# Kernel tuning notes

Hardware: AMD Instinct MI355X
Metric: run time of the kernel (lower is better)

The kernel has to match this reference:

```python
import jax, jax.numpy as jnp
import numpy as np

B, T = 16, 512
LAT, ACT, TSK = 512, 64, 96
E, NH, HD = 1024, 16, 64
L, HID, MAXS = 4, 4096, 512


def setup_inputs() -> dict:
    key = jax.random.key(0)
    ks = jax.random.split(key, 16)
    def rn(k, shape, std=0.02):
        return jax.random.normal(k, shape, jnp.float32) * std
    return {
        "z": jax.random.normal(ks[0], (B, T, LAT), jnp.float32),
        "a": jax.random.normal(ks[1], (B, T, ACT), jnp.float32),
        "task_emb": jax.random.normal(ks[2], (B, T, TSK), jnp.float32),
        "input_proj_w": rn(ks[3], (LAT + ACT + TSK, E)),
        "input_proj_b": jnp.zeros((E,), jnp.float32),
        "pos_emb": rn(ks[4], (1, MAXS, E)),
        "ln1_w": jnp.ones((L, E), jnp.float32),
        "ln1_b": jnp.zeros((L, E), jnp.float32),
        "qkv_w": rn(ks[5], (L, E, 3 * E)),
        "proj_w": rn(ks[6], (L, E, E)),
        "proj_b": jnp.zeros((L, E), jnp.float32),
        "ln2_w": jnp.ones((L, E), jnp.float32),
        "ln2_b": jnp.zeros((L, E), jnp.float32),
        "mlp_w1": rn(ks[7], (L, E, HID)),
        "mlp_b1": jnp.zeros((L, HID), jnp.float32),
        "mlp_w2": rn(ks[8], (L, HID, E)),
        "mlp_b2": jnp.zeros((L, E), jnp.float32),
        "out_norm_w": jnp.ones((E,), jnp.float32),
        "out_norm_b": jnp.zeros((E,), jnp.float32),
        "delta_w": rn(ks[9], (E, LAT)),
        "delta_b": jnp.zeros((LAT,), jnp.float32),
    }


def _ln(x, w, b, eps=1e-5):
    mu = jnp.mean(x, -1, keepdims=True)
    var = jnp.mean((x - mu) ** 2, -1, keepdims=True)
    return (x - mu) * jax.lax.rsqrt(var + eps) * w + b


def reference(z, a, task_emb, input_proj_w, input_proj_b, pos_emb,
              ln1_w, ln1_b, qkv_w, proj_w, proj_b, ln2_w, ln2_b,
              mlp_w1, mlp_b1, mlp_w2, mlp_b2,
              out_norm_w, out_norm_b, delta_w, delta_b):
    Bv, Tv, _ = z.shape
    x = jnp.concatenate([z, a, task_emb], axis=-1) @ input_proj_w + input_proj_b
    x = x + pos_emb[:, :Tv]
    scale = HD ** -0.5
    causal = jnp.tril(jnp.ones((Tv, Tv), bool))  # seq_start=0, no cache
    for l in range(L):
        h = _ln(x, ln1_w[l], ln1_b[l])
        qkv = (h @ qkv_w[l]).reshape(Bv, Tv, 3, NH, HD)
        q = jnp.swapaxes(qkv[:, :, 0], 1, 2) * scale  # (B,H,T,D)
        k = jnp.swapaxes(qkv[:, :, 1], 1, 2)
        v = jnp.swapaxes(qkv[:, :, 2], 1, 2)
        attn = jnp.einsum('bhqd,bhkd->bhqk', q, k)
        attn = jnp.where(causal, attn, -jnp.inf)
        attn = jax.nn.softmax(attn, axis=-1)
        o = jnp.einsum('bhqk,bhkd->bhqd', attn, v)
        o = jnp.swapaxes(o, 1, 2).reshape(Bv, Tv, E)
        x = x + (o @ proj_w[l] + proj_b[l])
        h2 = _ln(x, ln2_w[l], ln2_b[l])
        mid = jax.nn.gelu(h2 @ mlp_w1[l] + mlp_b1[l], approximate=False)
        x = x + (mid @ mlp_w2[l] + mlp_b2[l])
    x = _ln(x, out_norm_w, out_norm_b)
    return z + (x @ delta_w + delta_b)
```

## Files before the change

kernel.cpp:

```cpp
#include <hip/hip_runtime.h>
#include <hip/hip_bf16.h>
#include <math.h>

typedef unsigned short u16;
typedef unsigned int u32;
typedef __attribute__((ext_vector_type(4))) float f32x4;
typedef __attribute__((ext_vector_type(8))) short bf16x8;

#define DEV static __device__ __forceinline__

DEV u16 f2bf(float f) {
  __hip_bfloat16 h = __float2bfloat16(f);
  union { __hip_bfloat16 h; u16 u; } c; c.h = h; return c.u;
}

DEV float fast_gelu(float v) {
  float u = v * (1.5957691216f + 0.0713548162f * v * v);
  return v * __builtin_amdgcn_rcpf(1.f + __expf(-u));
}

DEV void gload16(const void* g, void* l) {
  __builtin_amdgcn_global_load_lds((const __attribute__((address_space(1))) u32*)g,
                                   (__attribute__((address_space(3))) u32*)l, 16, 0, 0);
}

__global__ void transpose_w(const float* __restrict__ src, u16* __restrict__ dst,
                            int R, int C, int Rp) {
  __shared__ float tile[32][33];
  int tx = threadIdx.x, ty = threadIdx.y;
  int c0 = blockIdx.x * 32, r0 = blockIdx.y * 32;
  #pragma unroll
  for (int j = 0; j < 4; j++) {
    int r = r0 + ty + j * 8, c = c0 + tx;
    tile[ty + j * 8][tx] = (r < R && c < C) ? src[(size_t)r * C + c] : 0.f;
  }
  __syncthreads();
  #pragma unroll
  for (int j = 0; j < 4; j++) {
    int cc = c0 + ty + j * 8;
    int rr = r0 + tx;
    if (cc < C && rr < Rp) dst[(size_t)cc * Rp + rr] = f2bf(tile[tx][ty + j * 8]);
  }
}

__global__ void concat_k(const float* __restrict__ z, const float* __restrict__ a,
                         const float* __restrict__ te, u16* __restrict__ A) {
  const int total = 8192 * 704;
  for (int idx = blockIdx.x * 256 + threadIdx.x; idx < total; idx += gridDim.x * 256) {
    int m = idx / 704;
    int j = idx - m * 704;
    float v = 0.f;
    if (j < 512) v = z[(size_t)m * 512 + j];
    else if (j < 576) v = a[(size_t)m * 64 + (j - 512)];
    else if (j < 672) v = te[(size_t)m * 96 + (j - 576)];
    A[idx] = f2bf(v);
  }
}

__global__ __launch_bounds__(256) void ln_k(const float* __restrict__ x,
                                            const float* __restrict__ w,
                                            const float* __restrict__ b,
                                            u16* __restrict__ h) {
  int row = blockIdx.x * 4 + (threadIdx.x >> 6);
  int lane = threadIdx.x & 63;
  const float4* xr = (const float4*)(x + (size_t)row * 1024);
  float4 v[4]; float s = 0.f, sq = 0.f;
  #pragma unroll
  for (int i = 0; i < 4; i++) {
    v[i] = xr[lane + i * 64];
    s += v[i].x + v[i].y + v[i].z + v[i].w;
    sq += v[i].x * v[i].x + v[i].y * v[i].y + v[i].z * v[i].z + v[i].w * v[i].w;
  }
  #pragma unroll
  for (int off = 32; off >= 1; off >>= 1) { s += __shfl_xor(s, off); sq += __shfl_xor(sq, off); }
  float mean = s * (1.f / 1024.f);
  float var = sq * (1.f / 1024.f) - mean * mean;
  float rstd = rsqrtf(var + 1e-5f);
  const float4* wv = (const float4*)w;
  const float4* bv = (const float4*)b;
  u32* hr = (u32*)(h + (size_t)row * 1024);
  #pragma unroll
  for (int i = 0; i < 4; i++) {
    int idx = lane + i * 64;
    float4 wi = wv[idx], bi = bv[idx];
    float o0 = (v[i].x - mean) * rstd * wi.x + bi.x;
    float o1 = (v[i].y - mean) * rstd * wi.y + bi.y;
    float o2 = (v[i].z - mean) * rstd * wi.z + bi.z;
    float o3 = (v[i].w - mean) * rstd * wi.w + bi.w;
    hr[idx * 2]     = (u32)f2bf(o0) | ((u32)f2bf(o1) << 16);
    hr[idx * 2 + 1] = (u32)f2bf(o2) | ((u32)f2bf(o3) << 16);
  }
}

template <int FM, int EPI>
__global__ __launch_bounds__(512, 2) void gemm8(
    const u16* __restrict__ A, const u16* __restrict__ BT,
    float* __restrict__ outF, u16* __restrict__ outH,
    const float* __restrict__ bias, const float* __restrict__ res,
    const float* __restrict__ pos, int M, int N, int K, int gx) {
  constexpr int BM = FM * 32;
  constexpr int ABYTES = BM * 64;
  constexpr int BBYTES = 256 * 64;
  constexpr int SLICE = ABYTES + BBYTES;
  constexpr int LA = ABYTES / 8192;
  constexpr int LB = 2;
  __shared__ char lds[4 * SLICE];

  const int tid = threadIdx.x, lane = tid & 63, w = tid >> 6;
  const int wr = w >> 2, wc = w & 3;

  const int nwg = gridDim.x, orig = blockIdx.x;
  const int q = nwg >> 3, r = nwg & 7;
  const int xcd = orig & 7, loc = orig >> 3;
  const int sid = (xcd < r ? xcd * (q + 1) : r * (q + 1) + (xcd - r) * q) + loc;
  const int m0 = (sid / gx) * BM, n0 = (sid % gx) * 256;

  const char* Ag = (const char*)(A + (size_t)m0 * K);
  const char* Bg = (const char*)(BT + (size_t)n0 * K);
  const int Krow = K * 2;

  int aoff[LA], boff[LB];
  #pragma unroll
  for (int l = 0; l < LA; l++) {
    int c = l * 512 + tid, rw = c >> 2, g = (c & 3) ^ ((rw >> 1) & 3);
    aoff[l] = rw * Krow + g * 16;
  }
  #pragma unroll
  for (int l = 0; l < LB; l++) {
    int c = l * 512 + tid, rw = c >> 2, g = (c & 3) ^ ((rw >> 1) & 3);
    boff[l] = rw * Krow + g * 16;
  }
  const int ra = wr * (FM * 16) + (lane & 15);
  const int aRd = ra * 64 + (((lane >> 4) ^ ((ra >> 1) & 3)) << 4);
  const int rb = wc * 64 + (lane & 15);
  const int bRd = rb * 64 + (((lane >> 4) ^ ((rb >> 1) & 3)) << 4);

  f32x4 zero4 = {0.f, 0.f, 0.f, 0.f};
  f32x4 acc[FM][4];
  #pragma unroll
  for (int m = 0; m < FM; m++)
    #pragma unroll
    for (int n = 0; n < 4; n++) acc[m][n] = zero4;

  auto stageA = [&](int s) {
    char* Ad = lds + (s & 3) * SLICE;
    const char* src = Ag + (size_t)s * 64;
    #pragma unroll
    for (int l = 0; l < LA; l++)
      gload16(src + aoff[l], Ad + (l * 512 + w * 64) * 16);
  };
  auto stageB = [&](int s) {
    char* Bd = lds + (s & 3) * SLICE + ABYTES;
    const char* src = Bg + (size_t)s * 64;
    #pragma unroll
    for (int l = 0; l < LB; l++)
      gload16(src + boff[l], Bd + (l * 512 + w * 64) * 16);
  };

  const int NS = K >> 5;
  stageA(0); stageB(0); stageA(1); stageB(1);
  asm volatile("s_waitcnt vmcnt(3)" ::: "memory");
  __builtin_amdgcn_s_barrier();

  #pragma unroll 1
  for (int s = 0; s < NS; s++) {
    char* Ar = lds + (s & 3) * SLICE;
    char* Br = Ar + ABYTES;
    const bool pre = (s + 2 < NS);
    bf16x8 bfr[4], af[4];
    #pragma unroll
    for (int n = 0; n < 4; n++) bfr[n] = *(const bf16x8*)(Br + bRd + n * 1024);
    #pragma unroll
    for (int m = 0; m < 4; m++) af[m] = *(const bf16x8*)(Ar + aRd + m * 1024);
    if (pre) { stageA(s + 2); stageB(s + 2); }
    __builtin_amdgcn_sched_barrier(0);
    __builtin_amdgcn_s_barrier();
    asm volatile("s_waitcnt lgkmcnt(0)" ::: "memory");
    __builtin_amdgcn_sched_barrier(0);
    __builtin_amdgcn_s_setprio(1);
    #pragma unroll
    for (int m = 0; m < 4; m++)
      #pragma unroll
      for (int n = 0; n < 4; n++)
        acc[m][n] = __builtin_amdgcn_mfma_f32_16x16x32_bf16(af[m], bfr[n], acc[m][n], 0, 0, 0);
    __builtin_amdgcn_s_setprio(0);
    __builtin_amdgcn_sched_barrier(0);
    if (pre) asm volatile("s_waitcnt vmcnt(3)" ::: "memory");
    else     asm volatile("s_waitcnt vmcnt(0)" ::: "memory");
    __builtin_amdgcn_s_barrier();
  }

  #pragma unroll
  for (int m = 0; m < FM; m++) {
    #pragma unroll
    for (int i = 0; i < 4; i++) {
      int gm = m0 + wr * (FM * 16) + m * 16 + ((lane >> 4) << 2) + i;
      #pragma unroll
      for (int n = 0; n < 4; n++) {
        int gn = n0 + wc * 64 + n * 16 + (lane & 15);
        float v = acc[m][n][i];
        if (EPI & 1) v += bias[gn];
        if (EPI & 2) v += pos[(size_t)(gm & 511) * N + gn];
        if (EPI & 4) v += res[(size_t)gm * N + gn];
        if (EPI & 8) v = fast_gelu(v);
        if (EPI & 16) outH[(size_t)gm * N + gn] = f2bf(v);
        else outF[(size_t)gm * N + gn] = v;
      }
    }
  }
}

#define SB0 __builtin_amdgcn_sched_barrier(0)
#define VMW(N) asm volatile("s_waitcnt vmcnt(" #N ")" ::: "memory")
#define PH_TAIL(MFMAS) \
  SB0; __builtin_amdgcn_s_barrier(); \
  asm volatile("s_waitcnt lgkmcnt(0)" ::: "memory"); SB0; \
  __builtin_amdgcn_s_setprio(1); MFMAS; __builtin_amdgcn_s_setprio(0); \
  SB0; __builtin_amdgcn_s_barrier();
#define PH_TAILV(MFMAS, NN) \
  SB0; __builtin_amdgcn_s_barrier(); \
  asm volatile("s_waitcnt lgkmcnt(0)" ::: "memory"); SB0; \
  __builtin_amdgcn_s_setprio(1); MFMAS; __builtin_amdgcn_s_setprio(0); \
  SB0; VMW(NN); __builtin_amdgcn_s_barrier();
#define MM16(MB, BF) \
  _Pragma("unroll") \
  for (int mm = 0; mm < 4; mm++) \
    _Pragma("unroll") \
    for (int nn = 0; nn < 4; nn++) \
      acc[(MB) + mm][nn] = __builtin_amdgcn_mfma_f32_16x16x32_bf16(afr[mm][0], BF[nn], acc[(MB) + mm][nn], 0, 0, 0);
#define MM32(MB) \
  _Pragma("unroll") \
  for (int kk2 = 0; kk2 < 2; kk2++) \
    _Pragma("unroll") \
    for (int mm = 0; mm < 4; mm++) \
      _Pragma("unroll") \
      for (int nn = 0; nn < 4; nn++) \
        acc[(MB) + mm][nn] = __builtin_amdgcn_mfma_f32_16x16x32_bf16( \
            afr[mm][kk2], kk2 ? bfr1[nn] : bfr0[nn], acc[(MB) + mm][nn], 0, 0, 0);
#define RD_A1(BUF, K2L, MB) { \
  const char* _b = aRdB[BUF]; \
  afr[0][0] = *(const bf16x8*)(_b + aby[(MB) + 0][K2L]); \
  afr[1][0] = *(const bf16x8*)(_b + aby[(MB) + 1][K2L]); \
  afr[2][0] = *(const bf16x8*)(_b + aby[(MB) + 2][K2L]); \
  afr[3][0] = *(const bf16x8*)(_b + aby[(MB) + 3][K2L]); }
#define RD_A8(BUF, MB) { \
  const char* _b = aRdB[BUF]; \
  afr[0][0] = *(const bf16x8*)(_b + aby[(MB) + 0][0]); \
  afr[0][1] = *(const bf16x8*)(_b + aby[(MB) + 0][1]); \
  afr[1][0] = *(const bf16x8*)(_b + aby[(MB) + 1][0]); \
  afr[1][1] = *(const bf16x8*)(_b + aby[(MB) + 1][1]); \
  afr[2][0] = *(const bf16x8*)(_b + aby[(MB) + 2][0]); \
  afr[2][1] = *(const bf16x8*)(_b + aby[(MB) + 2][1]); \
  afr[3][0] = *(const bf16x8*)(_b + aby[(MB) + 3][0]); \
  afr[3][1] = *(const bf16x8*)(_b + aby[(MB) + 3][1]); }
#define RD_BALL(BUF) { \
  const char* _b = bRdB[BUF]; \
  bfr0[0] = *(const bf16x8*)(_b + bby[0][0]); bfr1[0] = *(const bf16x8*)(_b + bby[0][1]); \
  bfr0[1] = *(const bf16x8*)(_b + bby[1][0]); bfr1[1] = *(const bf16x8*)(_b + bby[1][1]); \
  bfr0[2] = *(const bf16x8*)(_b + bby[2][0]); bfr1[2] = *(const bf16x8*)(_b + bby[2][1]); \
  bfr0[3] = *(const bf16x8*)(_b + bby[3][0]); bfr1[3] = *(const bf16x8*)(_b + bby[3][1]); }

template <int FM, int EPI>
__global__ __launch_bounds__(512, 2) void gemmP(
    const u16* __restrict__ A, const u16* __restrict__ BT,
    float* __restrict__ outF, u16* __restrict__ outH,
    const float* __restrict__ bias, const float* __restrict__ res,
    const float* __restrict__ pos, int M, int N, int K, int gx) {
  constexpr int RB = 16384;
  constexpr int NAREG = (FM == 8 ? 4 : 2);
  constexpr int BOFF = NAREG * RB;
  __shared__ char lds[BOFF + 4 * RB];

  const int tid = threadIdx.x, lane = tid & 63, w = tid >> 6;
  const int wr = w >> 2, wc = w & 3;
  const int ln = lane & 15, g = lane >> 4;

  const int nwg = gridDim.x, orig = blockIdx.x;
  const int q = nwg >> 3, r = nwg & 7;
  const int xcd = orig & 7, loc = orig >> 3;
  const int sid = (xcd < r ? xcd * (q + 1) : r * (q + 1) + (xcd - r) * q) + loc;
  const int m0 = (sid / gx) * (FM * 32), n0 = (sid % gx) * 256;

  const char* Ag = (const char*)(A + (size_t)m0 * K);
  const char* Bg = (const char*)(BT + (size_t)n0 * K);
  const size_t K2 = (size_t)K * 2;
  const int NT = K >> 6, NTm1 = NT - 1, NI = NT >> 1;

  int aby[FM][2], bby[4][2];
  #pragma unroll
  for (int m = 0; m < FM; m++) {
    int rr = (FM == 8 ? 0 : wr * 64) + m * 16 + ln;
    #pragma unroll
    for (int k2 = 0; k2 < 2; k2++)
      aby[m][k2] = rr * 128 + (((k2 * 4 + g) ^ (rr & 7)) << 4);
  }
  #pragma unroll
  for (int n = 0; n < 4; n++) {
    int rr = (wc & 1) * 64 + n * 16 + ln;
    #pragma unroll
    for (int k2 = 0; k2 < 2; k2++)
      bby[n][k2] = rr * 128 + (((k2 * 4 + g) ^ (rr & 7)) << 4);
  }
  const char* aRdB[2];
  const char* bRdB[2];
  if constexpr (FM == 8) {
    aRdB[0] = lds + (0 * 2 + wr) * RB;
    aRdB[1] = lds + (1 * 2 + wr) * RB;
  } else {
    aRdB[0] = lds;
    aRdB[1] = lds + RB;
  }
  bRdB[0] = lds + BOFF + (0 * 2 + (wc >> 1)) * RB;
  bRdB[1] = lds + BOFF + (1 * 2 + (wc >> 1)) * RB;

  int soff[2], sdst[2];
  #pragma unroll
  for (int l = 0; l < 2; l++) {
    int c = l * 512 + tid, rw = c >> 3, sl = c & 7;
    soff[l] = rw * (int)K2 + ((sl ^ (rw & 7)) << 4);
    sdst[l] = (l * 512 + w * 64) * 16;
  }

  auto stA = [&](int buf, int tau, int h) {
    char* d = lds + (FM == 8 ? (buf * 2 + h) : buf) * RB;
    const char* s = Ag + (size_t)(tau < NT ? tau : NTm1) * 128 + (FM == 8 ? (size_t)h * 128 * K2 : 0);
    #pragma unroll
    for (int l = 0; l < 2; l++) gload16(s + soff[l], d + sdst[l]);
  };
  auto stB = [&](int buf, int tau, int gg) {
    char* d = lds + BOFF + (buf * 2 + gg) * RB;
    const char* s = Bg + (size_t)(tau < NT ? tau : NTm1) * 128 + (size_t)gg * 128 * K2;
    #pragma unroll
    for (int l = 0; l < 2; l++) gload16(s + soff[l], d + sdst[l]);
  };

  f32x4 zero4 = {0.f, 0.f, 0.f, 0.f};
  f32x4 acc[FM][4];
  #pragma unroll
  for (int m = 0; m < FM; m++)
    #pragma unroll
    for (int n = 0; n < 4; n++) acc[m][n] = zero4;

  bf16x8 afr[4][2], bfr0[4], bfr1[4];

  if constexpr (FM == 8) {
    stA(0, 0, 0); stA(0, 0, 1); stB(0, 0, 0); stB(0, 0, 1); stB(1, 1, 0); stB(1, 1, 1);
    VMW(4);
    __builtin_amdgcn_s_barrier();
    #pragma unroll 1
    for (int J = 0; J < NI; J++) {
      const int t = 2 * J;
      RD_BALL(0); RD_A8(0, 0); stA(1, t + 1, 0); stA(1, t + 1, 1);
      PH_TAIL(MM32(0));
      RD_A8(0, 4); stB(0, t + 2, 0); stB(0, t + 2, 1);
      PH_TAILV(MM32(4), 4);
      RD_BALL(1); RD_A8(1, 0); stA(0, t + 2, 0); stA(0, t + 2, 1);
      PH_TAIL(MM32(0));
      RD_A8(1, 4); stB(1, t + 3, 0); stB(1, t + 3, 1);
      PH_TAILV(MM32(4), 4);
    }
  } else {
    stA(0, 0, 0); stB(0, 0, 0); stB(0, 0, 1); stB(1, 1, 0); stB(1, 1, 1);
    VMW(4);
    __builtin_amdgcn_s_barrier();
    #pragma unroll 1
    for (int J = 0; J < NI; J++) {
      const int t = 2 * J;
      RD_BALL(0); RD_A1(0, 0, 0); stA(1, t + 1, 0);
      PH_TAIL(MM16(0, bfr0));
      RD_A1(0, 1, 0); stB(0, t + 2, 0);
      PH_TAILV(MM16(0, bfr1), 2);
      RD_BALL(1); RD_A1(1, 0, 0); stB(0, t + 2, 1); stA(0, t + 2, 0);
      PH_TAIL(MM16(0, bfr0));
      RD_A1(1, 1, 0); stB(1, t + 3, 0); stB(1, t + 3, 1);
      PH_TAILV(MM16(0, bfr1), 4);
    }
  }
  VMW(0);

  #pragma unroll
  for (int m = 0; m < FM; m++) {
    #pragma unroll
    for (int i = 0; i < 4; i++) {
      int gm = m0 + wr * (FM * 16) + m * 16 + (g << 2) + i;
      #pragma unroll
      for (int n = 0; n < 4; n++) {
        int gn = n0 + wc * 64 + n * 16 + ln;
        float v = acc[m][n][i];
        if (EPI & 1) v += bias[gn];
        if (EPI & 2) v += pos[(size_t)(gm & 511) * N + gn];
        if (EPI & 4) v += res[(size_t)gm * N + gn];
        if (EPI & 8) v = fast_gelu(v);
        if (EPI & 16) outH[(size_t)gm * N + gn] = f2bf(v);
        else outF[(size_t)gm * N + gn] = v;
      }
    }
  }
}
#undef RD_BALL
#undef RD_A8
#undef RD_A1
#undef MM32
#undef MM16
#undef PH_TAILV
#undef PH_TAIL
#undef VMW
#undef SB0

__global__ __launch_bounds__(512) void attn_k(const u16* __restrict__ qkv,
                                              u16* __restrict__ o) {
  __shared__ u16 Ks[512 * 64];
  __shared__ u16 Vt[64 * 512];
  __shared__ u16 Ps[8 * 512];
  const int tid = threadIdx.x, lane = tid & 63, w = tid >> 6;
  const int b = blockIdx.x >> 4, h = blockIdx.x & 15;
  const u16* base = qkv + (size_t)b * 512 * 3072 + h * 64;

  #pragma unroll
  for (int it = 0; it < 8; it++) {
    int chunk = it * 512 + tid;
    int row = chunk >> 3;
    int ib = (chunk & 7) * 16;
    int lb = ib ^ ((row & 7) << 4);
    gload16((const char*)(base + 1024 + (size_t)row * 3072) + lb,
            (char*)Ks + (it * 512 + w * 64) * 16);
  }
  {
    const u16* vrow = base + 2048 + (size_t)tid * 3072;
    #pragma unroll
    for (int c = 0; c < 8; c++) {
      uint4 u = *(const uint4*)(vrow + c * 8);
      u32 vals[4] = {u.x, u.y, u.z, u.w};
      #pragma unroll
      for (int pcompo = 0; pcompo < 4; pcompo++) {
        int d0 = c * 8 + pcompo * 2;
        size_t by0 = ((size_t)d0 * 1024 + tid * 2) ^ (size_t)((d0 & 7) << 4);
        size_t by1 = ((size_t)(d0 + 1) * 1024 + tid * 2) ^ (size_t)(((d0 + 1) & 7) << 4);
        *(u16*)((char*)Vt + by0) = (u16)(vals[pcompo] & 0xffff);
        *(u16*)((char*)Vt + by1) = (u16)(vals[pcompo] >> 16);
      }
    }
  }
  __syncthreads();

  const int qts[4] = {w, 15 - w, 16 + w, 31 - w};
  #pragma unroll
  for (int qi = 0; qi < 4; qi++) {
    const int qt = qts[qi];
    const int q0 = qt * 16;
    const int qcol = q0 + (lane & 15);
    const u16* qrow = base + (size_t)(q0 + (lane & 15)) * 3072 + ((lane >> 4) << 3);
    bf16x8 qf0 = *(const bf16x8*)qrow;
    bf16x8 qf1 = *(const bf16x8*)(qrow + 32);
    f32x4 zero4 = {0.f, 0.f, 0.f, 0.f};
    f32x4 oA[4] = {zero4, zero4, zero4, zero4};
    float mrun = -INFINITY, lrun = 0.f;
    const int nch = (qt >> 1) + 1;
    for (int ch = 0; ch < nch; ch++) {
      const int kb = ch * 32;
      f32x4 st0 = zero4, st1 = zero4;
      {
        int krow = kb + (lane & 15);
        int byc = krow * 128 + ((lane >> 4) << 4);
        int sw = (krow & 7) << 4;
        bf16x8 ka = *(const bf16x8*)((const char*)Ks + (byc ^ sw));
        bf16x8 kb2 = *(const bf16x8*)((const char*)Ks + ((byc + 64) ^ sw));
        st0 = __builtin_amdgcn_mfma_f32_16x16x32_bf16(ka, qf0, st0, 0, 0, 0);
        st0 = __builtin_amdgcn_mfma_f32_16x16x32_bf16(kb2, qf1, st0, 0, 0, 0);
      }
      {
        int krow = kb + 16 + (lane & 15);
        int byc = krow * 128 + ((lane >> 4) << 4);
        int sw = (krow & 7) << 4;
        bf16x8 ka = *(const bf16x8*)((const char*)Ks + (byc ^ sw));
        bf16x8 kb2 = *(const bf16x8*)((const char*)Ks + ((byc + 64) ^ sw));
        st1 = __builtin_amdgcn_mfma_f32_16x16x32_bf16(ka, qf0, st1, 0, 0, 0);
        st1 = __builtin_amdgcn_mfma_f32_16x16x32_bf16(kb2, qf1, st1, 0, 0, 0);
      }
      float sv[8]; float cmax = -INFINITY;
      #pragma unroll
      for (int i = 0; i < 4; i++) {
        int key0 = kb + ((lane >> 4) << 2) + i;
        float s0 = st0[i] * 0.125f; if (key0 > qcol) s0 = -INFINITY;
        float s1 = st1[i] * 0.125f; if (key0 + 16 > qcol) s1 = -INFINITY;
        sv[i] = s0; sv[4 + i] = s1;
        cmax = fmaxf(cmax, fmaxf(s0, s1));
      }
      cmax = fmaxf(cmax, __shfl_xor(cmax, 16));
      cmax = fmaxf(cmax, __shfl_xor(cmax, 32));
      float mnew = fmaxf(mrun, cmax);
      float corr = __expf(mrun - mnew);
      float pp[8]; float psum = 0.f;
      #pragma unroll
      for (int i = 0; i < 8; i++) { pp[i] = __expf(sv[i] - mnew); psum += pp[i]; }
      psum += __shfl_xor(psum, 16);
      psum += __shfl_xor(psum, 32);
      lrun = lrun * corr + psum;
      mrun = mnew;
      {
        int rowq = lane & 15;
        int pbase = w * 1024 + rowq * 64;
        int sw = (rowq & 3) << 4;
        uint2 t0, t1;
        t0.x = (u32)f2bf(pp[0]) | ((u32)f2bf(pp[1]) << 16);
        t0.y = (u32)f2bf(pp[2]) | ((u32)f2bf(pp[3]) << 16);
        t1.x = (u32)f2bf(pp[4]) | ((u32)f2bf(pp[5]) << 16);
        t1.y = (u32)f2bf(pp[6]) | ((u32)f2bf(pp[7]) << 16);
        int off0 = (((lane >> 4) << 3)) ^ sw;
        int off1 = (32 + ((lane >> 4) << 3)) ^ sw;
        *(uint2*)((char*)Ps + pbase + off0) = t0;
        *(uint2*)((char*)Ps + pbase + off1) = t1;
      }
      #pragma unroll
      for (int i = 0; i < 4; i++) {
        float fi = __shfl(corr, ((lane >> 4) << 2) + i);
        oA[0][i] *= fi; oA[1][i] *= fi; oA[2][i] *= fi; oA[3][i] *= fi;
      }
      {
        int rowq = lane & 15;
        int pby = w * 1024 + rowq * 64 + ((((lane >> 4) << 4)) ^ ((rowq & 3) << 4));
        bf16x8 pf = *(const bf16x8*)((const char*)Ps + pby);
        #pragma unroll
        for (int n = 0; n < 4; n++) {
          int d = n * 16 + (lane & 15);
          int vby = (d * 1024 + (kb + ((lane >> 4) << 3)) * 2) ^ ((d & 7) << 4);
          bf16x8 vf = *(const bf16x8*)((const char*)Vt + vby);
          oA[n] = __builtin_amdgcn_mfma_f32_16x16x32_bf16(pf, vf, oA[n], 0, 0, 0);
        }
      }
    }
    float inv = 1.f / lrun;
    #pragma unroll
    for (int i = 0; i < 4; i++) {
      float fi = __shfl(inv, ((lane >> 4) << 2) + i);
      int qr = q0 + ((lane >> 4) << 2) + i;
      size_t orow = ((size_t)b * 512 + qr) * 1024 + h * 64;
      #pragma unroll
      for (int n = 0; n < 4; n++)
        o[orow + n * 16 + (lane & 15)] = f2bf(oA[n][i] * fi);
    }
  }
}

extern "C" void kernel_launch(void* const* d_in, const int* in_sizes, int n_in,
                              void* d_out, int out_size, void* d_ws, size_t ws_size,
                              hipStream_t stream) {
  const float* z    = (const float*)d_in[0];
  const float* a    = (const float*)d_in[1];
  const float* te   = (const float*)d_in[2];
  const float* ipw  = (const float*)d_in[3];
  const float* ipb  = (const float*)d_in[4];
  const float* pos  = (const float*)d_in[5];
  const float* ln1w = (const float*)d_in[6];
  const float* ln1b = (const float*)d_in[7];
  const float* qkvw = (const float*)d_in[8];
  const float* projw= (const float*)d_in[9];
  const float* projb= (const float*)d_in[10];
  const float* ln2w = (const float*)d_in[11];
  const float* ln2b = (const float*)d_in[12];
  const float* w1   = (const float*)d_in[13];
  const float* b1   = (const float*)d_in[14];
  const float* w2   = (const float*)d_in[15];
  const float* b2   = (const float*)d_in[16];
  const float* onw  = (const float*)d_in[17];
  const float* onb  = (const float*)d_in[18];
  const float* dw   = (const float*)d_in[19];
  const float* db   = (const float*)d_in[20];
  float* out = (float*)d_out;

  char* p = (char*)d_ws;
  auto alloc = [&](size_t bytes) -> char* {
    char* r = p; p += (bytes + 255) & ~(size_t)255; return r;
  };
  u16* wt_in   = (u16*)alloc((size_t)1024 * 704 * 2);
  u16* wt_qkv  = (u16*)alloc((size_t)4 * 3072 * 1024 * 2);
  u16* wt_proj = (u16*)alloc((size_t)4 * 1024 * 1024 * 2);
  u16* wt_m1   = (u16*)alloc((size_t)4 * 4096 * 1024 * 2);
  u16* wt_m2   = (u16*)alloc((size_t)4 * 1024 * 4096 * 2);
  u16* wt_d    = (u16*)alloc((size_t)512 * 1024 * 2);
  u16* abuf    = (u16*)alloc((size_t)8192 * 704 * 2);
  float* xbuf  = (float*)alloc((size_t)8192 * 1024 * 4);
  u16* hbuf    = (u16*)alloc((size_t)8192 * 1024 * 2);
  u16* big     = (u16*)alloc((size_t)8192 * 4096 * 2);
  u16* obuf    = (u16*)alloc((size_t)8192 * 1024 * 2);
  u16* qkvb = big;
  u16* mid  = big;

  dim3 tb(32, 8);
  auto TR = [&](const float* s, u16* d, int R, int C, int Rp) {
    dim3 g((C + 31) / 32, (Rp + 31) / 32);
    transpose_w<<<g, tb, 0, stream>>>(s, d, R, C, Rp);
  };
  TR(ipw, wt_in, 672, 1024, 704);
  for (int l = 0; l < 4; l++) TR(qkvw + (size_t)l * 1024 * 3072, wt_qkv + (size_t)l * 3072 * 1024, 1024, 3072, 1024);
  for (int l = 0; l < 4; l++) TR(projw + (size_t)l * 1024 * 1024, wt_proj + (size_t)l * 1024 * 1024, 1024, 1024, 1024);
  for (int l = 0; l < 4; l++) TR(w1 + (size_t)l * 1024 * 4096, wt_m1 + (size_t)l * 4096 * 1024, 1024, 4096, 1024);
  for (int l = 0; l < 4; l++) TR(w2 + (size_t)l * 4096 * 1024, wt_m2 + (size_t)l * 1024 * 4096, 4096, 1024, 4096);
  TR(dw, wt_d, 1024, 512, 1024);

  concat_k<<<4096, 256, 0, stream>>>(z, a, te, abuf);

  gemm8<4, 3><<<4 * 64, 512, 0, stream>>>(abuf, wt_in, xbuf, nullptr, ipb, nullptr, pos, 8192, 1024, 704, 4);

  for (int l = 0; l < 4; l++) {
    ln_k<<<2048, 256, 0, stream>>>(xbuf, ln1w + l * 1024, ln1b + l * 1024, hbuf);
    gemmP<8, 16><<<384, 512, 0, stream>>>(hbuf, wt_qkv + (size_t)l * 3072 * 1024, nullptr, qkvb, nullptr, nullptr, nullptr, 8192, 3072, 1024, 12);
    attn_k<<<256, 512, 0, stream>>>(qkvb, obuf);
    gemmP<4, 5><<<256, 512, 0, stream>>>(obuf, wt_proj + (size_t)l * 1024 * 1024, xbuf, nullptr, projb + l * 1024, xbuf, nullptr, 8192, 1024, 1024, 4);
    ln_k<<<2048, 256, 0, stream>>>(xbuf, ln2w + l * 1024, ln2b + l * 1024, hbuf);
    gemmP<8, 25><<<512, 512, 0, stream>>>(hbuf, wt_m1 + (size_t)l * 4096 * 1024, nullptr, mid, b1 + l * 4096, nullptr, nullptr, 8192, 4096, 1024, 16);
    gemmP<4, 5><<<256, 512, 0, stream>>>(mid, wt_m2 + (size_t)l * 1024 * 4096, xbuf, nullptr, b2 + l * 1024, xbuf, nullptr, 8192, 1024, 4096, 4);
  }
  ln_k<<<2048, 256, 0, stream>>>(xbuf, onw, onb, hbuf);
  gemmP<4, 5><<<128, 512, 0, stream>>>(hbuf, wt_d, out, nullptr, db, z, nullptr, 8192, 512, 1024, 2);
}
```

Measured before the change: 1.372 ms.

## Restructure GEMM main loop into two-phase double-buffered pipeline with split LDS waits

Replaces the four-phase-per-iteration GEMM schedule, which had two barriers per phase and B tiles prefetched two steps ahead, with a simpler double-buffered scheme. Each half-iteration now waits on all outstanding global loads, takes a single barrier, issues the next tile's global-to-LDS loads, and reads all A/B fragments for the current tile. A partial lgkmcnt wait lets the first MFMA group start before the second group's fragments arrive. This cuts barrier count and serialisation between phases, but shortens the prefetch distance and adds extra fragment registers (afr1), which risks exposed memory latency or register pressure.

New measurement: 1.375 ms. About the same (+0.2%).

```diff
diff --git a/kernel.cpp b/kernel.cpp
--- a/kernel.cpp
+++ b/kernel.cpp
@@ -211,24 +211,10 @@
 }
 
 #define SB0 __builtin_amdgcn_sched_barrier(0)
-#define VMW(N) asm volatile("s_waitcnt vmcnt(" #N ")" ::: "memory")
-#define PH_TAIL(MFMAS) \
-  SB0; __builtin_amdgcn_s_barrier(); \
-  asm volatile("s_waitcnt lgkmcnt(0)" ::: "memory"); SB0; \
-  __builtin_amdgcn_s_setprio(1); MFMAS; __builtin_amdgcn_s_setprio(0); \
-  SB0; __builtin_amdgcn_s_barrier();
-#define PH_TAILV(MFMAS, NN) \
-  SB0; __builtin_amdgcn_s_barrier(); \
-  asm volatile("s_waitcnt lgkmcnt(0)" ::: "memory"); SB0; \
-  __builtin_amdgcn_s_setprio(1); MFMAS; __builtin_amdgcn_s_setprio(0); \
-  SB0; VMW(NN); __builtin_amdgcn_s_barrier();
-#define MM16(MB, BF) \
-  _Pragma("unroll") \
-  for (int mm = 0; mm < 4; mm++) \
-    _Pragma("unroll") \
-    for (int nn = 0; nn < 4; nn++) \
-      acc[(MB) + mm][nn] = __builtin_amdgcn_mfma_f32_16x16x32_bf16(afr[mm][0], BF[nn], acc[(MB) + mm][nn], 0, 0, 0);
-#define MM32(MB) \
+#define VMW0 asm volatile("s_waitcnt vmcnt(0)" ::: "memory")
+#define LGKM8 asm volatile("s_waitcnt lgkmcnt(8)" ::: "memory")
+#define LGKM0 asm volatile("s_waitcnt lgkmcnt(0)" ::: "memory")
+#define MM32A(AF, MB) \
   _Pragma("unroll") \
   for (int kk2 = 0; kk2 < 2; kk2++) \
     _Pragma("unroll") \
@@ -236,29 +222,38 @@
       _Pragma("unroll") \
       for (int nn = 0; nn < 4; nn++) \
         acc[(MB) + mm][nn] = __builtin_amdgcn_mfma_f32_16x16x32_bf16( \
-            afr[mm][kk2], kk2 ? bfr1[nn] : bfr0[nn], acc[(MB) + mm][nn], 0, 0, 0);
-#define RD_A1(BUF, K2L, MB) { \
-  const char* _b = aRdB[BUF]; \
-  afr[0][0] = *(const bf16x8*)(_b + aby[(MB) + 0][K2L]); \
-  afr[1][0] = *(const bf16x8*)(_b + aby[(MB) + 1][K2L]); \
-  afr[2][0] = *(const bf16x8*)(_b + aby[(MB) + 2][K2L]); \
-  afr[3][0] = *(const bf16x8*)(_b + aby[(MB) + 3][K2L]); }
-#define RD_A8(BUF, MB) { \
-  const char* _b = aRdB[BUF]; \
-  afr[0][0] = *(const bf16x8*)(_b + aby[(MB) + 0][0]); \
-  afr[0][1] = *(const bf16x8*)(_b + aby[(MB) + 0][1]); \
-  afr[1][0] = *(const bf16x8*)(_b + aby[(MB) + 1][0]); \
-  afr[1][1] = *(const bf16x8*)(_b + aby[(MB) + 1][1]); \
-  afr[2][0] = *(const bf16x8*)(_b + aby[(MB) + 2][0]); \
-  afr[2][1] = *(const bf16x8*)(_b + aby[(MB) + 2][1]); \
-  afr[3][0] = *(const bf16x8*)(_b + aby[(MB) + 3][0]); \
-  afr[3][1] = *(const bf16x8*)(_b + aby[(MB) + 3][1]); }
-#define RD_BALL(BUF) { \
+            AF[mm][kk2], kk2 ? bfr1[nn] : bfr0[nn], acc[(MB) + mm][nn], 0, 0, 0);
+#define MM16K(KL) \
+  _Pragma("unroll") \
+  for (int mm = 0; mm < 4; mm++) \
+    _Pragma("unroll") \
+    for (int nn = 0; nn < 4; nn++) \
+      acc[mm][nn] = __builtin_amdgcn_mfma_f32_16x16x32_bf16( \
+          afr0[mm][KL], KL ? bfr1[nn] : bfr0[nn], acc[mm][nn], 0, 0, 0);
+#define RD_B2(BUF) { \
   const char* _b = bRdB[BUF]; \
   bfr0[0] = *(const bf16x8*)(_b + bby[0][0]); bfr1[0] = *(const bf16x8*)(_b + bby[0][1]); \
   bfr0[1] = *(const bf16x8*)(_b + bby[1][0]); bfr1[1] = *(const bf16x8*)(_b + bby[1][1]); \
   bfr0[2] = *(const bf16x8*)(_b + bby[2][0]); bfr1[2] = *(const bf16x8*)(_b + bby[2][1]); \
   bfr0[3] = *(const bf16x8*)(_b + bby[3][0]); bfr1[3] = *(const bf16x8*)(_b + bby[3][1]); }
+#define RD_A4(BUF, MB, DST) { \
+  const char* _b = aRdB[BUF]; \
+  DST[0][0] = *(const bf16x8*)(_b + aby[(MB) + 0][0]); DST[0][1] = *(const bf16x8*)(_b + aby[(MB) + 0][1]); \
+  DST[1][0] = *(const bf16x8*)(_b + aby[(MB) + 1][0]); DST[1][1] = *(const bf16x8*)(_b + aby[(MB) + 1][1]); \
+  DST[2][0] = *(const bf16x8*)(_b + aby[(MB) + 2][0]); DST[2][1] = *(const bf16x8*)(_b + aby[(MB) + 2][1]); \
+  DST[3][0] = *(const bf16x8*)(_b + aby[(MB) + 3][0]); DST[3][1] = *(const bf16x8*)(_b + aby[(MB) + 3][1]); }
+#define RD_BK(BUF, KL, DST4) { \
+  const char* _b = bRdB[BUF]; \
+  DST4[0] = *(const bf16x8*)(_b + bby[0][KL]); \
+  DST4[1] = *(const bf16x8*)(_b + bby[1][KL]); \
+  DST4[2] = *(const bf16x8*)(_b + bby[2][KL]); \
+  DST4[3] = *(const bf16x8*)(_b + bby[3][KL]); }
+#define RD_AK(BUF, KL) { \
+  const char* _b = aRdB[BUF]; \
+  afr0[0][KL] = *(const bf16x8*)(_b + aby[0][KL]); \
+  afr0[1][KL] = *(const bf16x8*)(_b + aby[1][KL]); \
+  afr0[2][KL] = *(const bf16x8*)(_b + aby[2][KL]); \
+  afr0[3][KL] = *(const bf16x8*)(_b + aby[3][KL]); }
 
 template <int FM, int EPI>
 __global__ __launch_bounds__(512, 2) void gemmP(
@@ -341,42 +336,58 @@
     #pragma unroll
     for (int n = 0; n < 4; n++) acc[m][n] = zero4;
 
-  bf16x8 afr[4][2], bfr0[4], bfr1[4];
+  bf16x8 afr0[4][2], afr1[4][2], bfr0[4], bfr1[4];
 
   if constexpr (FM == 8) {
-    stA(0, 0, 0); stA(0, 0, 1); stB(0, 0, 0); stB(0, 0, 1); stB(1, 1, 0); stB(1, 1, 1);
-    VMW(4);
-    __builtin_amdgcn_s_barrier();
+    stA(0, 0, 0); stA(0, 0, 1); stB(0, 0, 0); stB(0, 0, 1);
     #pragma unroll 1
     for (int J = 0; J < NI; J++) {
       const int t = 2 * J;
-      RD_BALL(0); RD_A8(0, 0); stA(1, t + 1, 0); stA(1, t + 1, 1);
-      PH_TAIL(MM32(0));
-      RD_A8(0, 4); stB(0, t + 2, 0); stB(0, t + 2, 1);
-      PH_TAILV(MM32(4), 4);
-      RD_BALL(1); RD_A8(1, 0); stA(0, t + 2, 0); stA(0, t + 2, 1);
-      PH_TAIL(MM32(0));
-      RD_A8(1, 4); stB(1, t + 3, 0); stB(1, t + 3, 1);
-      PH_TAILV(MM32(4), 4);
+      VMW0; SB0;
+      __builtin_amdgcn_s_barrier();
+      stA(1, t + 1, 0); stA(1, t + 1, 1); stB(1, t + 1, 0); stB(1, t + 1, 1);
+      RD_B2(0); RD_A4(0, 0, afr0); SB0;
+      RD_A4(0, 4, afr1); SB0;
+      LGKM8; SB0;
+      __builtin_amdgcn_s_setprio(1); MM32A(afr0, 0); __builtin_amdgcn_s_setprio(0); SB0;
+      LGKM0; SB0;
+      __builtin_amdgcn_s_setprio(1); MM32A(afr1, 4); __builtin_amdgcn_s_setprio(0); SB0;
+      VMW0; SB0;
+      __builtin_amdgcn_s_barrier();
+      stA(0, t + 2, 0); stA(0, t + 2, 1); stB(0, t + 2, 0); stB(0, t + 2, 1);
+      RD_B2(1); RD_A4(1, 0, afr0); SB0;
+      RD_A4(1, 4, afr1); SB0;
+      LGKM8; SB0;
+      __builtin_amdgcn_s_setprio(1); MM32A(afr0, 0); __builtin_amdgcn_s_setprio(0); SB0;
+      LGKM0; SB0;
+      __builtin_amdgcn_s_setprio(1); MM32A(afr1, 4); __builtin_amdgcn_s_setprio(0); SB0;
     }
   } else {
-    stA(0, 0, 0); stB(0, 0, 0); stB(0, 0, 1); stB(1, 1, 0); stB(1, 1, 1);
-    VMW(4);
-    __builtin_amdgcn_s_barrier();
+    stA(0, 0, 0); stB(0, 0, 0); stB(0, 0, 1);
     #pragma unroll 1
     for (int J = 0; J < NI; J++) {
       const int t = 2 * J;
-      RD_BALL(0); RD_A1(0, 0, 0); stA(1, t + 1, 0);
-      PH_TAIL(MM16(0, bfr0));
-      RD_A1(0, 1, 0); stB(0, t + 2, 0);
-      PH_TAILV(MM16(0, bfr1), 2);
-      RD_BALL(1); RD_A1(1, 0, 0); stB(0, t + 2, 1); stA(0, t + 2, 0);
-      PH_TAIL(MM16(0, bfr0));
-      RD_A1(1, 1, 0); stB(1, t + 3, 0); stB(1, t + 3, 1);
-      PH_TAILV(MM16(0, bfr1), 4);
+      VMW0; SB0;
+      __builtin_amdgcn_s_barrier();
+      stA(1, t + 1, 0); stB(1, t + 1, 0); stB(1, t + 1, 1);
+      RD_BK(0, 0, bfr0); RD_AK(0, 0); SB0;
+      RD_BK(0, 1, bfr1); RD_AK(0, 1); SB0;
+      LGKM8; SB0;
+      __builtin_amdgcn_s_setprio(1); MM16K(0); __builtin_amdgcn_s_setprio(0); SB0;
+      LGKM0; SB0;
+      __builtin_amdgcn_s_setprio(1); MM16K(1); __builtin_amdgcn_s_setprio(0); SB0;
+      VMW0; SB0;
+      __builtin_amdgcn_s_barrier();
+      stA(0, t + 2, 0); stB(0, t + 2, 0); stB(0, t + 2, 1);
+      RD_BK(1, 0, bfr0); RD_AK(1, 0); SB0;
+      RD_BK(1, 1, bfr1); RD_AK(1, 1); SB0;
+      LGKM8; SB0;
+      __builtin_amdgcn_s_setprio(1); MM16K(0); __builtin_amdgcn_s_setprio(0); SB0;
+      LGKM0; SB0;
+      __builtin_amdgcn_s_setprio(1); MM16K(1); __builtin_amdgcn_s_setprio(0); SB0;
     }
   }
-  VMW(0);
+  VMW0;
 
   #pragma unroll
   for (int m = 0; m < FM; m++) {
@@ -397,14 +408,15 @@
     }
   }
 }
-#undef RD_BALL
-#undef RD_A8
-#undef RD_A1
-#undef MM32
-#undef MM16
-#undef PH_TAILV
-#undef PH_TAIL
-#undef VMW
+#undef RD_AK
+#undef RD_BK
+#undef RD_A4
+#undef RD_B2
+#undef MM16K
+#undef MM32A
+#undef LGKM0
+#undef LGKM8
+#undef VMW0
 #undef SB0
 
 __global__ __launch_bounds__(512) void attn_k(const u16* __restrict__ qkv,
```

## Widen attention key chunks to 64 and batch weight transposes across layers

Applied to the files above, without the earlier changes.

The attention kernel now handles 64 keys per online-softmax step instead of 32. This halves the number of max/sum shuffle reductions and correction rescales, and doubles the P staging buffer in shared memory. Separately, the per-layer weight transpose launches are merged into one launch per weight type using blockIdx.z with strides, which cuts launch count. The cost is more registers per thread in attention and coarser causal chunks, so more masked work is done on the diagonal tiles.

After: 1.334 ms. -2.7%, faster.

```diff
diff --git a/kernel.cpp b/kernel.cpp
--- a/kernel.cpp
+++ b/kernel.cpp
@@ -25,7 +25,9 @@
 }
 
 __global__ void transpose_w(const float* __restrict__ src, u16* __restrict__ dst,
-                            int R, int C, int Rp) {
+                            int R, int C, int Rp, size_t sstride, size_t dstride) {
+  src += (size_t)blockIdx.z * sstride;
+  dst += (size_t)blockIdx.z * dstride;
   __shared__ float tile[32][33];
   int tx = threadIdx.x, ty = threadIdx.y;
   int c0 = blockIdx.x * 32, r0 = blockIdx.y * 32;
@@ -411,10 +413,11 @@
                                               u16* __restrict__ o) {
   __shared__ u16 Ks[512 * 64];
   __shared__ u16 Vt[64 * 512];
-  __shared__ u16 Ps[8 * 512];
+  __shared__ u16 Ps[8 * 1024];
   const int tid = threadIdx.x, lane = tid & 63, w = tid >> 6;
   const int b = blockIdx.x >> 4, h = blockIdx.x & 15;
   const u16* base = qkv + (size_t)b * 512 * 3072 + h * 64;
+  const int ln = lane & 15, g = lane >> 4;
 
   #pragma unroll
   for (int it = 0; it < 8; it++) {
@@ -432,12 +435,12 @@
       uint4 u = *(const uint4*)(vrow + c * 8);
       u32 vals[4] = {u.x, u.y, u.z, u.w};
       #pragma unroll
-      for (int pcompo = 0; pcompo < 4; pcompo++) {
-        int d0 = c * 8 + pcompo * 2;
+      for (int pc = 0; pc < 4; pc++) {
+        int d0 = c * 8 + pc * 2;
         size_t by0 = ((size_t)d0 * 1024 + tid * 2) ^ (size_t)((d0 & 7) << 4);
         size_t by1 = ((size_t)(d0 + 1) * 1024 + tid * 2) ^ (size_t)(((d0 + 1) & 7) << 4);
-        *(u16*)((char*)Vt + by0) = (u16)(vals[pcompo] & 0xffff);
-        *(u16*)((char*)Vt + by1) = (u16)(vals[pcompo] >> 16);
+        *(u16*)((char*)Vt + by0) = (u16)(vals[pc] & 0xffff);
+        *(u16*)((char*)Vt + by1) = (u16)(vals[pc] >> 16);
       }
     }
   }
@@ -448,96 +451,95 @@
   for (int qi = 0; qi < 4; qi++) {
     const int qt = qts[qi];
     const int q0 = qt * 16;
-    const int qcol = q0 + (lane & 15);
-    const u16* qrow = base + (size_t)(q0 + (lane & 15)) * 3072 + ((lane >> 4) << 3);
+    const int qcol = q0 + ln;
+    const u16* qrow = base + (size_t)(q0 + ln) * 3072 + (g << 3);
     bf16x8 qf0 = *(const bf16x8*)qrow;
     bf16x8 qf1 = *(const bf16x8*)(qrow + 32);
     f32x4 zero4 = {0.f, 0.f, 0.f, 0.f};
     f32x4 oA[4] = {zero4, zero4, zero4, zero4};
     float mrun = -INFINITY, lrun = 0.f;
-    const int nch = (qt >> 1) + 1;
+    const int nch = (qt >> 2) + 1;
     for (int ch = 0; ch < nch; ch++) {
-      const int kb = ch * 32;
-      f32x4 st0 = zero4, st1 = zero4;
-      {
-        int krow = kb + (lane & 15);
-        int byc = krow * 128 + ((lane >> 4) << 4);
+      const int kb = ch * 64;
+      f32x4 st[4];
+      #pragma unroll
+      for (int s = 0; s < 4; s++) {
+        st[s] = zero4;
+        int krow = kb + s * 16 + ln;
+        int byc = krow * 128 + (g << 4);
         int sw = (krow & 7) << 4;
-        bf16x8 ka = *(const bf16x8*)((const char*)Ks + (byc ^ sw));
+        bf16x8 ka  = *(const bf16x8*)((const char*)Ks + (byc ^ sw));
         bf16x8 kb2 = *(const bf16x8*)((const char*)Ks + ((byc + 64) ^ sw));
-        st0 = __builtin_amdgcn_mfma_f32_16x16x32_bf16(ka, qf0, st0, 0, 0, 0);
-        st0 = __builtin_amdgcn_mfma_f32_16x16x32_bf16(kb2, qf1, st0, 0, 0, 0);
-      }
-      {
-        int krow = kb + 16 + (lane & 15);
-        int byc = krow * 128 + ((lane >> 4) << 4);
-        int sw = (krow & 7) << 4;
-        bf16x8 ka = *(const bf16x8*)((const char*)Ks + (byc ^ sw));
-        bf16x8 kb2 = *(const bf16x8*)((const char*)Ks + ((byc + 64) ^ sw));
-        st1 = __builtin_amdgcn_mfma_f32_16x16x32_bf16(ka, qf0, st1, 0, 0, 0);
-        st1 = __builtin_amdgcn_mfma_f32_16x16x32_bf16(kb2, qf1, st1, 0, 0, 0);
-      }
-      float sv[8]; float cmax = -INFINITY;
-      #pragma unroll
-      for (int i = 0; i < 4; i++) {
-        int key0 = kb + ((lane >> 4) << 2) + i;
-        float s0 = st0[i] * 0.125f; if (key0 > qcol) s0 = -INFINITY;
-        float s1 = st1[i] * 0.125f; if (key0 + 16 > qcol) s1 = -INFINITY;
-        sv[i] = s0; sv[4 + i] = s1;
-        cmax = fmaxf(cmax, fmaxf(s0, s1));
+        st[s] = __builtin_amdgcn_mfma_f32_16x16x32_bf16(ka, qf0, st[s], 0, 0, 0);
+        st[s] = __builtin_amdgcn_mfma_f32_16x16x32_bf16(kb2, qf1, st[s], 0, 0, 0);
+      }
+      float sv[16]; float cmax = -INFINITY;
+      #pragma unroll
+      for (int s = 0; s < 4; s++) {
+        #pragma unroll
+        for (int i = 0; i < 4; i++) {
+          int key0 = kb + s * 16 + (g << 2) + i;
+          float v = st[s][i] * 0.125f;
+          if (key0 > qcol) v = -INFINITY;
+          sv[s * 4 + i] = v;
+          cmax = fmaxf(cmax, v);
+        }
       }
       cmax = fmaxf(cmax, __shfl_xor(cmax, 16));
       cmax = fmaxf(cmax, __shfl_xor(cmax, 32));
       float mnew = fmaxf(mrun, cmax);
       float corr = __expf(mrun - mnew);
-      float pp[8]; float psum = 0.f;
-      #pragma unroll
-      for (int i = 0; i < 8; i++) { pp[i] = __expf(sv[i] - mnew); psum += pp[i]; }
+      float pp[16]; float psum = 0.f;
+      #pragma unroll
+      for (int i = 0; i < 16; i++) { pp[i] = __expf(sv[i] - mnew); psum += pp[i]; }
       psum += __shfl_xor(psum, 16);
       psum += __shfl_xor(psum, 32);
       lrun = lrun * corr + psum;
       mrun = mnew;
       {
-        int rowq = lane & 15;
-        int pbase = w * 1024 + rowq * 64;
-        int sw = (rowq & 3) << 4;
-        uint2 t0, t1;
-        t0.x = (u32)f2bf(pp[0]) | ((u32)f2bf(pp[1]) << 16);
-        t0.y = (u32)f2bf(pp[2]) | ((u32)f2bf(pp[3]) << 16);
-        t1.x = (u32)f2bf(pp[4]) | ((u32)f2bf(pp[5]) << 16);
-        t1.y = (u32)f2bf(pp[6]) | ((u32)f2bf(pp[7]) << 16);
-        int off0 = (((lane >> 4) << 3)) ^ sw;
-        int off1 = (32 + ((lane >> 4) << 3)) ^ sw;
-        *(uint2*)((char*)Ps + pbase + off0) = t0;
-        *(uint2*)((char*)Ps + pbase + off1) = t1;
+        int sw2 = (ln & 3) << 4;
+        #pragma unroll
+        for (int hh = 0; hh < 2; hh++) {
+          int pbase = w * 2048 + hh * 1024 + ln * 64;
+          uint2 t0, t1;
+          t0.x = (u32)f2bf(pp[8 * hh + 0]) | ((u32)f2bf(pp[8 * hh + 1]) << 16);
+          t0.y = (u32)f2bf(pp[8 * hh + 2]) | ((u32)f2bf(pp[8 * hh + 3]) << 16);
+          t1.x = (u32)f2bf(pp[8 * hh + 4]) | ((u32)f2bf(pp[8 * hh + 5]) << 16);
+          t1.y = (u32)f2bf(pp[8 * hh + 6]) | ((u32)f2bf(pp[8 * hh + 7]) << 16);
+          *(uint2*)((char*)Ps + pbase + ((g << 3) ^ sw2)) = t0;
+          *(uint2*)((char*)Ps + pbase + ((32 + (g << 3)) ^ sw2)) = t1;
+        }
       }
       #pragma unroll
       for (int i = 0; i < 4; i++) {
-        float fi = __shfl(corr, ((lane >> 4) << 2) + i);
+        float fi = __shfl(corr, (g << 2) + i);
         oA[0][i] *= fi; oA[1][i] *= fi; oA[2][i] *= fi; oA[3][i] *= fi;
       }
       {
-        int rowq = lane & 15;
-        int pby = w * 1024 + rowq * 64 + ((((lane >> 4) << 4)) ^ ((rowq & 3) << 4));
-        bf16x8 pf = *(const bf16x8*)((const char*)Ps + pby);
+        int sw2 = (ln & 3) << 4;
         #pragma unroll
-        for (int n = 0; n < 4; n++) {
-          int d = n * 16 + (lane & 15);
-          int vby = (d * 1024 + (kb + ((lane >> 4) << 3)) * 2) ^ ((d & 7) << 4);
-          bf16x8 vf = *(const bf16x8*)((const char*)Vt + vby);
-          oA[n] = __builtin_amdgcn_mfma_f32_16x16x32_bf16(pf, vf, oA[n], 0, 0, 0);
+        for (int hh = 0; hh < 2; hh++) {
+          bf16x8 pf = *(const bf16x8*)((const char*)Ps + w * 2048 + hh * 1024 +
+                                       ln * 64 + ((g << 4) ^ sw2));
+          #pragma unroll
+          for (int n = 0; n < 4; n++) {
+            int d = n * 16 + ln;
+            int vby = (d * 1024 + (kb + 32 * hh + (g << 3)) * 2) ^ ((d & 7) << 4);
+            bf16x8 vf = *(const bf16x8*)((const char*)Vt + vby);
+            oA[n] = __builtin_amdgcn_mfma_f32_16x16x32_bf16(pf, vf, oA[n], 0, 0, 0);
+          }
         }
       }
     }
     float inv = 1.f / lrun;
     #pragma unroll
     for (int i = 0; i < 4; i++) {
-      float fi = __shfl(inv, ((lane >> 4) << 2) + i);
-      int qr = q0 + ((lane >> 4) << 2) + i;
+      float fi = __shfl(inv, (g << 2) + i);
+      int qr = q0 + (g << 2) + i;
       size_t orow = ((size_t)b * 512 + qr) * 1024 + h * 64;
       #pragma unroll
       for (int n = 0; n < 4; n++)
-        o[orow + n * 16 + (lane & 15)] = f2bf(oA[n][i] * fi);
+        o[orow + n * 16 + ln] = f2bf(oA[n][i] * fi);
     }
   }
 }
@@ -587,16 +589,16 @@
   u16* mid  = big;
 
   dim3 tb(32, 8);
-  auto TR = [&](const float* s, u16* d, int R, int C, int Rp) {
-    dim3 g((C + 31) / 32, (Rp + 31) / 32);
-    transpose_w<<<g, tb, 0, stream>>>(s, d, R, C, Rp);
-  };
-  TR(ipw, wt_in, 672, 1024, 704);
-  for (int l = 0; l < 4; l++) TR(qkvw + (size_t)l * 1024 * 3072, wt_qkv + (size_t)l * 3072 * 1024, 1024, 3072, 1024);
-  for (int l = 0; l < 4; l++) TR(projw + (size_t)l * 1024 * 1024, wt_proj + (size_t)l * 1024 * 1024, 1024, 1024, 1024);
-  for (int l = 0; l < 4; l++) TR(w1 + (size_t)l * 1024 * 4096, wt_m1 + (size_t)l * 4096 * 1024, 1024, 4096, 1024);
-  for (int l = 0; l < 4; l++) TR(w2 + (size_t)l * 4096 * 1024, wt_m2 + (size_t)l * 1024 * 4096, 4096, 1024, 4096);
-  TR(dw, wt_d, 1024, 512, 1024);
+  transpose_w<<<dim3(32, 22, 1), tb, 0, stream>>>(ipw, wt_in, 672, 1024, 704, 0, 0);
+  transpose_w<<<dim3(96, 32, 4), tb, 0, stream>>>(qkvw, wt_qkv, 1024, 3072, 1024,
+      (size_t)1024 * 3072, (size_t)3072 * 1024);
+  transpose_w<<<dim3(32, 32, 4), tb, 0, stream>>>(projw, wt_proj, 1024, 1024, 1024,
+      (size_t)1024 * 1024, (size_t)1024 * 1024);
+  transpose_w<<<dim3(128, 32, 4), tb, 0, stream>>>(w1, wt_m1, 1024, 4096, 1024,
+      (size_t)1024 * 4096, (size_t)4096 * 1024);
+  transpose_w<<<dim3(32, 128, 4), tb, 0, stream>>>(w2, wt_m2, 4096, 1024, 4096,
+      (size_t)4096 * 1024, (size_t)1024 * 4096);
+  transpose_w<<<dim3(16, 32, 1), tb, 0, stream>>>(dw, wt_d, 1024, 512, 1024, 0, 0);
 
   concat_k<<<4096, 256, 0, stream>>>(z, a, te, abuf);
 
```
